# Kernel tuning notes

Hardware: AMD Instinct MI355X
Metric: run time of the kernel (lower is better)

Reference implementation:

```python
import jax, jax.numpy as jnp
import numpy as np

SIGMA = 0.1   # sigma_disc (params[3])
ALPHA = 0.05  # alpha_disc (params[2])


def setup_inputs() -> dict:
    key = jax.random.key(0)
    k1, k2, k3 = jax.random.split(key, 3)
    E, S, T = 3, 8192, 100  # num_events, num_samples, num_bin + num_extra_bin
    logits = jax.random.normal(k1, (E, S, T), dtype=jnp.float32)
    event_out = jax.nn.softmax(logits, axis=-1)  # per-event discrete hazard probs, rows sum to 1
    event_times = jax.random.randint(k2, (S, E), 0, 99).astype(jnp.int32)
    labs = jax.random.randint(k3, (S, E), 0, 2).astype(jnp.int32)
    return {"event_out": event_out, "event_times": event_times, "labs": labs,
            "num_bin": 96, "num_extra_bin": 4}


def _c_loss(event_out, event_times, labs, T):
    # cum[e, k, t] = sum(event_out[e, k, :t+1]); risk with cutoff c = 1 - cum[..., c-1]
    cum = jnp.cumsum(event_out, axis=-1)  # (E, S, T)
    E = event_out.shape[0]
    penalty = jnp.float32(0.0)
    for i in range(E):  # small fixed number of events
        c = cum[i]                    # (S, T)
        t = event_times[:, i]         # (S,)
        lab = labs[:, i]              # (S,)
        had = lab == 1
        # ---- forward concordance (had_event branch) ----
        e_f = jnp.minimum(t + 1, T - 1)              # per-reference-sample cutoff, >= 1
        # risk_f[j, k] = 1 - sum(event_out[k, :e_f[j]]) = 1 - cum[k, e_f[j]-1]
        risk_f = 1.0 - c[:, e_f - 1].T               # (S_j, S_k)
        diff_f = risk_f - jnp.diagonal(risk_f)[:, None]  # comp_risk - reference_risk
        # f_compare: t_k > e_j - 1  OR  (t_k == e_j - 1 AND lab_k == 0)
        mask_f = had[:, None] & ((t[None, :] >= e_f[:, None]) |
                                 ((t[None, :] == e_f[:, None] - 1) & (lab[None, :] == 0)))
        penalty = penalty + jnp.sum(jnp.where(mask_f & (diff_f < 0),
                                              jnp.exp(-diff_f / SIGMA), 0.0))
        # ---- backward concordance (back_c branch, active when t_j > 0) ----
        e_b = jnp.minimum(jnp.where(had, t, t + 1), T - 1)
        risk_b = 1.0 - c[:, jnp.maximum(e_b, 1) - 1].T
        diff_b = risk_b - jnp.diagonal(risk_b)[:, None]
        # b_compare: t_k <= e_j - 1 AND lab_k == 1
        mask_b = (t > 0)[:, None] & (t[None, :] <= e_b[:, None] - 1) & (lab[None, :] == 1)
        penalty = penalty + jnp.sum(jnp.where(mask_b & (diff_b > 0),
                                              jnp.exp(diff_b / SIGMA), 0.0))
    return ALPHA * penalty


def reference(event_out, event_times, labs, num_bin, num_extra_bin):
    return _c_loss(event_out, event_times, labs, num_bin + num_extra_bin)
```

## Files before the change

kernel.cpp:

```cpp
#include <hip/hip_runtime.h>

#define E_CONST 3
#define T_CONST 100
#define C10 10.0f
#define ALPHA_C 0.05f
#define SPLIT 4

__device__ inline int waveInclScan(int v, int lane) {
    #pragma unroll
    for (int off = 1; off < 64; off <<= 1) {
        int n = __shfl_up(v, off, 64);
        if (lane >= off) v += n;
    }
    return v;
}

__global__ __launch_bounds__(256) void combo_kernel(
    const float* __restrict__ event_out, const int* __restrict__ et,
    const int* __restrict__ labs, float* __restrict__ cumT,
    int* __restrict__ perm, int* __restrict__ permB,
    int* __restrict__ binStartA, int* __restrict__ b1endA,
    int prepBlocks, int S)
{
    __shared__ float tile[64][101];
    __shared__ int histK[2 * T_CONST];
    __shared__ int histB[T_CONST];
    __shared__ int cursK[2 * T_CONST];
    __shared__ int cursB[T_CONST];
    __shared__ int wsK[4], wsB[4];

    const int tid = threadIdx.x;

    if ((int)blockIdx.x < prepBlocks) {
        const int rowbase = (int)blockIdx.x * 64;
        const float4* __restrict__ src =
            reinterpret_cast<const float4*>(event_out) + (size_t)rowbase * 25;
        for (int idx = tid; idx < 64 * 25; idx += 256) {
            const float4 v = src[idx];
            const int r = idx / 25;
            const int c = idx - r * 25;
            float* d = &tile[r][c * 4];
            d[0] = v.x; d[1] = v.y; d[2] = v.z; d[3] = v.w;
        }
        __syncthreads();
        if (tid < 64) {
            float run = 0.f;
            #pragma unroll 4
            for (int c = 0; c < T_CONST; ++c) { run += tile[tid][c]; tile[tid][c] = run; }
        }
        __syncthreads();
        const int i  = rowbase / S;
        const int s0 = rowbase - i * S;
        float* __restrict__ dst = cumT + (size_t)i * T_CONST * S + s0;
        for (int idx = tid; idx < 64 * T_CONST; idx += 256) {
            const int t = idx >> 6;
            const int r = idx & 63;
            dst[(size_t)t * S + r] = tile[r][t];
        }
        return;
    }

    const int i = (int)blockIdx.x - prepBlocks;
    const int lane = tid & 63, wid = tid >> 6;

    for (int b = tid; b < 2 * T_CONST; b += 256) histK[b] = 0;
    for (int b = tid; b < T_CONST; b += 256) histB[b] = 0;
    __syncthreads();

    for (int s0 = tid; s0 < S; s0 += 1024) {
        const int sB = s0 + 256, sC = s0 + 512, sD = s0 + 768;
        const int tA = et[s0 * E_CONST + i];
        const int lA = labs[s0 * E_CONST + i];
        int tB = 0, lB = 0, tC = 0, lC = 0, tD = 0, lD = 0;
        if (sB < S) { tB = et[sB * E_CONST + i]; lB = labs[sB * E_CONST + i]; }
        if (sC < S) { tC = et[sC * E_CONST + i]; lC = labs[sC * E_CONST + i]; }
        if (sD < S) { tD = et[sD * E_CONST + i]; lD = labs[sD * E_CONST + i]; }
        atomicAdd(&histK[tA * 2 + (1 - lA)], 1); if (lA) atomicAdd(&histB[tA], 1);
        if (sB < S) { atomicAdd(&histK[tB * 2 + (1 - lB)], 1); if (lB) atomicAdd(&histB[tB], 1); }
        if (sC < S) { atomicAdd(&histK[tC * 2 + (1 - lC)], 1); if (lC) atomicAdd(&histB[tC], 1); }
        if (sD < S) { atomicAdd(&histK[tD * 2 + (1 - lD)], 1); if (lD) atomicAdd(&histB[tD], 1); }
    }
    __syncthreads();

    const int vK = (tid < 2 * T_CONST) ? histK[tid] : 0;
    int inclK = waveInclScan(vK, lane);
    const int vB = (tid < T_CONST) ? histB[tid] : 0;
    int inclB = waveInclScan(vB, lane);
    if (lane == 63) { wsK[wid] = inclK; wsB[wid] = inclB; }
    __syncthreads();
    int offK = 0, offB = 0;
    for (int w = 0; w < wid; ++w) { offK += wsK[w]; offB += wsB[w]; }
    inclK += offK; inclB += offB;
    const int exclK = inclK - vK;
    const int exclB = inclB - vB;

    if (tid < 2 * T_CONST) {
        cursK[tid] = exclK;
        binStartA[i * 2 * T_CONST + tid] = exclK;
    }
    if (tid < T_CONST) {
        cursB[tid] = exclB;
        b1endA[i * T_CONST + tid] = inclB;
    }
    __syncthreads();

    for (int s0 = tid; s0 < S; s0 += 1024) {
        const int sB = s0 + 256, sC = s0 + 512, sD = s0 + 768;
        const int tA = et[s0 * E_CONST + i];
        const int lA = labs[s0 * E_CONST + i];
        int tB = 0, lB = 0, tC = 0, lC = 0, tD = 0, lD = 0;
        if (sB < S) { tB = et[sB * E_CONST + i]; lB = labs[sB * E_CONST + i]; }
        if (sC < S) { tC = et[sC * E_CONST + i]; lC = labs[sC * E_CONST + i]; }
        if (sD < S) { tD = et[sD * E_CONST + i]; lD = labs[sD * E_CONST + i]; }

        int slot = atomicAdd(&cursK[tA * 2 + (1 - lA)], 1);
        perm[i * S + slot] = s0;
        if (lA) { const int sb = atomicAdd(&cursB[tA], 1); permB[i * S + sb] = s0; }
        if (sB < S) {
            slot = atomicAdd(&cursK[tB * 2 + (1 - lB)], 1);
            perm[i * S + slot] = sB;
            if (lB) { const int sb = atomicAdd(&cursB[tB], 1); permB[i * S + sb] = sB; }
        }
        if (sC < S) {
            slot = atomicAdd(&cursK[tC * 2 + (1 - lC)], 1);
            perm[i * S + slot] = sC;
            if (lC) { const int sb = atomicAdd(&cursB[tC], 1); permB[i * S + sb] = sC; }
        }
        if (sD < S) {
            slot = atomicAdd(&cursK[tD * 2 + (1 - lD)], 1);
            perm[i * S + slot] = sD;
            if (lD) { const int sb = atomicAdd(&cursB[tD], 1); permB[i * S + sb] = sD; }
        }
    }
}

__global__ __launch_bounds__(256) void grouppair_kernel(
    const float* __restrict__ cumT, const int* __restrict__ perm,
    const int* __restrict__ permB, const int* __restrict__ binStartA,
    const int* __restrict__ b1endA, float* __restrict__ partials, int S)
{
    __shared__ __align__(16) float elds[2048];
    __shared__ float wsum[4];
    const int tid = threadIdx.x;

    int x = (int)blockIdx.x;
    const int sp = x & (SPLIT - 1); x >>= 2;
    const int dir = x & 1;          x >>= 1;
    const int tt = x % T_CONST;
    const int i  = x / T_CONST;

    const int* __restrict__ bs = binStartA + i * 2 * T_CONST;
    int kbeg, kend, rbeg, rlen, colIdx;
    if (dir == 0) {
        const int t = tt;
        kbeg = bs[2 * t];
        kend = bs[2 * t + 1];
        rbeg = kend;
        rlen = S - rbeg;
        colIdx = t;
    } else {
        const int cb = (T_CONST - 2) - tt;
        if (cb < 0) { if (tid == 0) partials[blockIdx.x] = 0.f; return; }
        kbeg = (cb == 0) ? bs[2] : bs[2 * cb + 1];
        kend = bs[2 * cb + 3];
        rbeg = 0;
        rlen = b1endA[i * T_CONST + cb];
        colIdx = cb;
    }
    const int K = kend - kbeg;
    if (K <= 0 || rlen <= 0) { if (tid == 0) partials[blockIdx.x] = 0.f; return; }

    const int qbeg = rbeg + (rlen * sp) / SPLIT;
    const int qend = rbeg + (rlen * (sp + 1)) / SPLIT;
    const int qn   = qend - qbeg;
    const int qnp  = (qn + 3) & ~3;

    const float* __restrict__ col = cumT + ((size_t)i * T_CONST + colIdx) * S;
    const int* __restrict__ pidx = (dir == 0 ? perm : permB) + i * S;
    const float sgn = (dir == 0) ? C10 : -C10;

    for (int idx = tid; idx < qnp; idx += 256) {
        float e = 0.f;
        if (idx < qn) e = __expf(sgn * col[pidx[qbeg + idx]]);
        elds[idx] = e;
    }
    __syncthreads();

    const int kq = tid & 31;
    const int ep = tid >> 5;
    const int qn4 = qnp >> 2;
    const float4* __restrict__ e4 = reinterpret_cast<const float4*>(elds);
    const int permBase = i * S;
    float blocktot = 0.f;
    const int nkc = (K + 31) >> 5;

    for (int kc = 0; kc < nkc; ++kc) {
        const int j = kbeg + (kc << 5) + kq;
        float thr = 1e30f, factor = 0.f;
        if (j < kend) {
            const float tval = __expf(C10 * col[perm[permBase + j]]);
            if (dir == 0) { thr = tval;          factor = 1.0f / tval; }
            else          { thr = 1.0f / tval;   factor = tval; }
        }
        float acc = 0.f;
        for (int q = ep; q < qn4; q += 8) {
            const float4 v = e4[q];
            acc += (v.x > thr) ? v.x : 0.f;
            acc += (v.y > thr) ? v.y : 0.f;
            acc += (v.z > thr) ? v.z : 0.f;
            acc += (v.w > thr) ? v.w : 0.f;
        }
        blocktot += acc * factor;
    }

    for (int off = 32; off > 0; off >>= 1) blocktot += __shfl_down(blocktot, off, 64);
    const int lane = tid & 63, wid = tid >> 6;
    if (lane == 0) wsum[wid] = blocktot;
    __syncthreads();
    if (tid == 0) partials[blockIdx.x] = wsum[0] + wsum[1] + wsum[2] + wsum[3];
}

__global__ __launch_bounds__(1024) void reduce_kernel(
    const float* __restrict__ partials, int n, float* __restrict__ out)
{
    const int tid = threadIdx.x;
    float s0 = 0.f, s1 = 0.f, s2 = 0.f, s3 = 0.f;
    const int n4 = n & ~3;
    for (int idx = tid * 4; idx < n4; idx += 4096) {
        const float4 v = *reinterpret_cast<const float4*>(partials + idx);
        s0 += v.x; s1 += v.y; s2 += v.z; s3 += v.w;
    }
    for (int idx = n4 + tid; idx < n; idx += 1024) s0 += partials[idx];
    float sum = (s0 + s1) + (s2 + s3);
    for (int off = 32; off > 0; off >>= 1) sum += __shfl_down(sum, off, 64);
    __shared__ float wsum[16];
    const int lane = tid & 63, wd = tid >> 6;
    if (lane == 0) wsum[wd] = sum;
    __syncthreads();
    if (tid == 0) {
        float t = 0.f;
        for (int w = 0; w < 16; ++w) t += wsum[w];
        out[0] = ALPHA_C * t;
    }
}

__global__ __launch_bounds__(64) void prep_fb_kernel(
    const float* __restrict__ event_out, const int* __restrict__ et,
    const int* __restrict__ labs, float* __restrict__ cumT,
    int* __restrict__ tlA, int S)
{
    const int gid = blockIdx.x * 64 + threadIdx.x;
    const int i = gid / S;
    const int s = gid - i * S;
    const float4* __restrict__ row =
        reinterpret_cast<const float4*>(event_out + (size_t)gid * T_CONST);
    float* __restrict__ base = cumT + (size_t)i * T_CONST * S + s;
    float run = 0.f;
    #pragma unroll
    for (int c = 0; c < T_CONST / 4; ++c) {
        const float4 v = row[c];
        const float c0 = run + v.x;
        const float c1 = c0 + v.y;
        const float c2 = c1 + v.z;
        const float c3 = c2 + v.w;
        base[(size_t)(4 * c + 0) * S] = c0;
        base[(size_t)(4 * c + 1) * S] = c1;
        base[(size_t)(4 * c + 2) * S] = c2;
        base[(size_t)(4 * c + 3) * S] = c3;
        run = c3;
    }
    const int t   = et[s * E_CONST + i];
    const int lab = labs[s * E_CONST + i];
    tlA[i * S + s] = (t & 0xffff) | (lab << 16);
}

__global__ __launch_bounds__(256) void pair_fb_kernel(
    const float* __restrict__ cumT, const int* __restrict__ tlA,
    float* __restrict__ partials, int S)
{
    const int bx = blockIdx.x;
    const int i = bx / S;
    const int k = bx - i * S;
    const int base = i * S;
    const int tlk = tlA[base + k];
    const int t_k = tlk & 0xffff;
    const int lab_k = tlk >> 16;
    const bool doF = (lab_k == 1);
    const bool doB = (t_k > 0);
    float sum = 0.f;
    if (doF || doB) {
        const int cb = lab_k ? (t_k > 0 ? t_k - 1 : 0) : t_k;
        const float* __restrict__ colF = cumT + ((size_t)i * T_CONST + t_k) * S;
        const float* __restrict__ colB = cumT + ((size_t)i * T_CONST + cb)  * S;
        const float vf_k = colF[k];
        const float vb_k = colB[k];
        const int* __restrict__ tlp = tlA + base;
        for (int s = threadIdx.x; s < S; s += 256) {
            const int tls = tlp[s];
            const int t_s = tls & 0xffff;
            const int lab_s = tls >> 16;
            if (doF) {
                const float vs = colF[s];
                const bool c = (t_s > t_k) | ((t_s == t_k) & (lab_s == 0));
                if (c & (vs > vf_k)) sum += __expf((vs - vf_k) * C10);
            }
            if (doB) {
                const float vs = colB[s];
                const bool c = (t_s <= cb) & (lab_s == 1);
                if (c & (vb_k > vs)) sum += __expf((vb_k - vs) * C10);
            }
        }
    }
    for (int off = 32; off > 0; off >>= 1) sum += __shfl_down(sum, off, 64);
    __shared__ float wsum[4];
    const int lane = threadIdx.x & 63, wd = threadIdx.x >> 6;
    if (lane == 0) wsum[wd] = sum;
    __syncthreads();
    if (threadIdx.x == 0) partials[bx] = wsum[0] + wsum[1] + wsum[2] + wsum[3];
}

extern "C" void kernel_launch(void* const* d_in, const int* in_sizes, int n_in,
                              void* d_out, int out_size, void* d_ws, size_t ws_size,
                              hipStream_t stream)
{
    const float* event_out = (const float*)d_in[0];
    const int*   et        = (const int*)d_in[1];
    const int*   labsp     = (const int*)d_in[2];
    const int S = in_sizes[1] / E_CONST;

    const size_t colElems = (size_t)E_CONST * T_CONST * S;
    const size_t esElems  = (size_t)E_CONST * S;
    const int    gpBlocks = E_CONST * T_CONST * 2 * SPLIT;

    char* p = (char*)d_ws;
    float* cumT     = (float*)p; p += colElems * 4;
    int*   perm     = (int*)p;   p += esElems * 4;
    int*   permB    = (int*)p;   p += esElems * 4;
    int*   binStart = (int*)p;   p += (size_t)E_CONST * 2 * T_CONST * 4;
    int*   b1end    = (int*)p;   p += (size_t)E_CONST * T_CONST * 4;
    float* partials = (float*)p; p += (size_t)gpBlocks * 4;
    const size_t needed = (size_t)(p - (char*)d_ws);
    const size_t fallback_needed = colElems * 4 + esElems * 4 * 2;

    const int prepBlocks = (E_CONST * S) / 64;

    if (ws_size >= needed && (E_CONST * S) % 64 == 0) {
        hipLaunchKernelGGL(combo_kernel, dim3(prepBlocks + E_CONST), dim3(256), 0, stream,
                           event_out, et, labsp, cumT, perm, permB,
                           binStart, b1end, prepBlocks, S);
        hipLaunchKernelGGL(grouppair_kernel, dim3(gpBlocks), dim3(256), 0, stream,
                           cumT, perm, permB, binStart, b1end, partials, S);
        hipLaunchKernelGGL(reduce_kernel, dim3(1), dim3(1024), 0, stream,
                           partials, gpBlocks, (float*)d_out);
    } else if (ws_size >= fallback_needed) {
        const int nB = E_CONST * S;
        float* cumT2     = (float*)d_ws;
        int*   tlA2      = (int*)(cumT2 + colElems);
        float* partials2 = (float*)(tlA2 + esElems);
        hipLaunchKernelGGL(prep_fb_kernel, dim3(E_CONST * S / 64), dim3(64), 0, stream,
                           event_out, et, labsp, cumT2, tlA2, S);
        hipLaunchKernelGGL(pair_fb_kernel, dim3(nB), dim3(256), 0, stream,
                           cumT2, tlA2, partials2, S);
        hipLaunchKernelGGL(reduce_kernel, dim3(1), dim3(1024), 0, stream,
                           partials2, nB, (float*)d_out);
    }
}
```

Measured before the change: 114.4 us.

## Register-block four references per thread and fold final reduction into pair kernel

In the pair kernel each thread now compares four reference thresholds against every exp value it reads from LDS. This reuses each shared-memory load four times, but the k chunk grows from 32 to 128. The separate reduce kernel launch is replaced by a last-block reduction using an atomic counter that the prep kernel resets. The prep/combo kernel also moves to 512-thread blocks. The cost is that, with roughly 40 samples per bin, many of the 128 k slots are padding with a 1e30 threshold, so compare work per useful pair can rise.

```diff
diff --git a/kernel.cpp b/kernel.cpp
--- a/kernel.cpp
+++ b/kernel.cpp
@@ -15,27 +15,28 @@
     return v;
 }
 
-__global__ __launch_bounds__(256) void combo_kernel(
+__global__ __launch_bounds__(512) void combo_kernel(
     const float* __restrict__ event_out, const int* __restrict__ et,
     const int* __restrict__ labs, float* __restrict__ cumT,
     int* __restrict__ perm, int* __restrict__ permB,
     int* __restrict__ binStartA, int* __restrict__ b1endA,
-    int prepBlocks, int S)
+    int* __restrict__ cnt, int prepBlocks, int S)
 {
     __shared__ float tile[64][101];
     __shared__ int histK[2 * T_CONST];
     __shared__ int histB[T_CONST];
     __shared__ int cursK[2 * T_CONST];
     __shared__ int cursB[T_CONST];
-    __shared__ int wsK[4], wsB[4];
+    __shared__ int wsK[8], wsB[8];
 
     const int tid = threadIdx.x;
 
     if ((int)blockIdx.x < prepBlocks) {
+        if (blockIdx.x == 0 && tid == 0) *cnt = 0;
         const int rowbase = (int)blockIdx.x * 64;
         const float4* __restrict__ src =
             reinterpret_cast<const float4*>(event_out) + (size_t)rowbase * 25;
-        for (int idx = tid; idx < 64 * 25; idx += 256) {
+        for (int idx = tid; idx < 64 * 25; idx += 512) {
             const float4 v = src[idx];
             const int r = idx / 25;
             const int c = idx - r * 25;
@@ -52,7 +53,7 @@
         const int i  = rowbase / S;
         const int s0 = rowbase - i * S;
         float* __restrict__ dst = cumT + (size_t)i * T_CONST * S + s0;
-        for (int idx = tid; idx < 64 * T_CONST; idx += 256) {
+        for (int idx = tid; idx < 64 * T_CONST; idx += 512) {
             const int t = idx >> 6;
             const int r = idx & 63;
             dst[(size_t)t * S + r] = tile[r][t];
@@ -63,12 +64,12 @@
     const int i = (int)blockIdx.x - prepBlocks;
     const int lane = tid & 63, wid = tid >> 6;
 
-    for (int b = tid; b < 2 * T_CONST; b += 256) histK[b] = 0;
-    for (int b = tid; b < T_CONST; b += 256) histB[b] = 0;
-    __syncthreads();
-
-    for (int s0 = tid; s0 < S; s0 += 1024) {
-        const int sB = s0 + 256, sC = s0 + 512, sD = s0 + 768;
+    for (int b = tid; b < 2 * T_CONST; b += 512) histK[b] = 0;
+    for (int b = tid; b < T_CONST; b += 512) histB[b] = 0;
+    __syncthreads();
+
+    for (int s0 = tid; s0 < S; s0 += 2048) {
+        const int sB = s0 + 512, sC = s0 + 1024, sD = s0 + 1536;
         const int tA = et[s0 * E_CONST + i];
         const int lA = labs[s0 * E_CONST + i];
         int tB = 0, lB = 0, tC = 0, lC = 0, tD = 0, lD = 0;
@@ -104,8 +105,8 @@
     }
     __syncthreads();
 
-    for (int s0 = tid; s0 < S; s0 += 1024) {
-        const int sB = s0 + 256, sC = s0 + 512, sD = s0 + 768;
+    for (int s0 = tid; s0 < S; s0 += 2048) {
+        const int sB = s0 + 512, sC = s0 + 1024, sD = s0 + 1536;
         const int tA = et[s0 * E_CONST + i];
         const int lA = labs[s0 * E_CONST + i];
         int tB = 0, lB = 0, tC = 0, lC = 0, tD = 0, lD = 0;
@@ -137,10 +138,12 @@
 __global__ __launch_bounds__(256) void grouppair_kernel(
     const float* __restrict__ cumT, const int* __restrict__ perm,
     const int* __restrict__ permB, const int* __restrict__ binStartA,
-    const int* __restrict__ b1endA, float* __restrict__ partials, int S)
+    const int* __restrict__ b1endA, float* __restrict__ partials,
+    int* __restrict__ cnt, float* __restrict__ out, int S, int nBlocks)
 {
     __shared__ __align__(16) float elds[2048];
     __shared__ float wsum[4];
+    __shared__ int lastFlag;
     const int tid = threadIdx.x;
 
     int x = (int)blockIdx.x;
@@ -150,74 +153,111 @@
     const int i  = x / T_CONST;
 
     const int* __restrict__ bs = binStartA + i * 2 * T_CONST;
-    int kbeg, kend, rbeg, rlen, colIdx;
+    int kbeg = 0, kend = 0, rbeg = 0, rlen = 0, colIdx = 0;
+    bool active = true;
     if (dir == 0) {
-        const int t = tt;
-        kbeg = bs[2 * t];
-        kend = bs[2 * t + 1];
+        kbeg = bs[2 * tt];
+        kend = bs[2 * tt + 1];
         rbeg = kend;
         rlen = S - rbeg;
-        colIdx = t;
+        colIdx = tt;
     } else {
         const int cb = (T_CONST - 2) - tt;
-        if (cb < 0) { if (tid == 0) partials[blockIdx.x] = 0.f; return; }
-        kbeg = (cb == 0) ? bs[2] : bs[2 * cb + 1];
-        kend = bs[2 * cb + 3];
-        rbeg = 0;
-        rlen = b1endA[i * T_CONST + cb];
-        colIdx = cb;
+        if (cb < 0) active = false;
+        else {
+            kbeg = (cb == 0) ? bs[2] : bs[2 * cb + 1];
+            kend = bs[2 * cb + 3];
+            rbeg = 0;
+            rlen = b1endA[i * T_CONST + cb];
+            colIdx = cb;
+        }
     }
     const int K = kend - kbeg;
-    if (K <= 0 || rlen <= 0) { if (tid == 0) partials[blockIdx.x] = 0.f; return; }
-
-    const int qbeg = rbeg + (rlen * sp) / SPLIT;
-    const int qend = rbeg + (rlen * (sp + 1)) / SPLIT;
-    const int qn   = qend - qbeg;
-    const int qnp  = (qn + 3) & ~3;
-
-    const float* __restrict__ col = cumT + ((size_t)i * T_CONST + colIdx) * S;
-    const int* __restrict__ pidx = (dir == 0 ? perm : permB) + i * S;
-    const float sgn = (dir == 0) ? C10 : -C10;
-
-    for (int idx = tid; idx < qnp; idx += 256) {
-        float e = 0.f;
-        if (idx < qn) e = __expf(sgn * col[pidx[qbeg + idx]]);
-        elds[idx] = e;
-    }
-    __syncthreads();
-
-    const int kq = tid & 31;
-    const int ep = tid >> 5;
-    const int qn4 = qnp >> 2;
-    const float4* __restrict__ e4 = reinterpret_cast<const float4*>(elds);
-    const int permBase = i * S;
+    if (K <= 0 || rlen <= 0) active = false;
+
     float blocktot = 0.f;
-    const int nkc = (K + 31) >> 5;
-
-    for (int kc = 0; kc < nkc; ++kc) {
-        const int j = kbeg + (kc << 5) + kq;
-        float thr = 1e30f, factor = 0.f;
-        if (j < kend) {
-            const float tval = __expf(C10 * col[perm[permBase + j]]);
-            if (dir == 0) { thr = tval;          factor = 1.0f / tval; }
-            else          { thr = 1.0f / tval;   factor = tval; }
-        }
-        float acc = 0.f;
-        for (int q = ep; q < qn4; q += 8) {
-            const float4 v = e4[q];
-            acc += (v.x > thr) ? v.x : 0.f;
-            acc += (v.y > thr) ? v.y : 0.f;
-            acc += (v.z > thr) ? v.z : 0.f;
-            acc += (v.w > thr) ? v.w : 0.f;
-        }
-        blocktot += acc * factor;
+    if (active) {
+        const int qbeg = rbeg + (rlen * sp) / SPLIT;
+        const int qend = rbeg + (rlen * (sp + 1)) / SPLIT;
+        const int qn   = qend - qbeg;
+        const int qnp  = (qn + 3) & ~3;
+
+        const float* __restrict__ col = cumT + ((size_t)i * T_CONST + colIdx) * S;
+        const int* __restrict__ pidx = (dir == 0 ? perm : permB) + i * S;
+        const float sgn = (dir == 0) ? C10 : -C10;
+
+        for (int idx = tid; idx < qnp; idx += 256) {
+            float e = 0.f;
+            if (idx < qn) e = __expf(sgn * col[pidx[qbeg + idx]]);
+            elds[idx] = e;
+        }
+        __syncthreads();
+
+        const int kq4 = (tid & 31) * 4;
+        const int ep  = tid >> 5;
+        const int qn4 = qnp >> 2;
+        const float4* __restrict__ e4 = reinterpret_cast<const float4*>(elds);
+        const int permBase = i * S;
+        const int nkc = (K + 127) >> 7;
+
+        for (int kc = 0; kc < nkc; ++kc) {
+            const int jb = kbeg + (kc << 7) + kq4;
+            float thr0 = 1e30f, thr1 = 1e30f, thr2 = 1e30f, thr3 = 1e30f;
+            float f0 = 0.f, f1 = 0.f, f2 = 0.f, f3 = 0.f;
+            if (jb + 0 < kend) { const float tv = __expf(C10 * col[perm[permBase + jb + 0]]);
+                if (dir == 0) { thr0 = tv; f0 = 1.0f / tv; } else { thr0 = 1.0f / tv; f0 = tv; } }
+            if (jb + 1 < kend) { const float tv = __expf(C10 * col[perm[permBase + jb + 1]]);
+                if (dir == 0) { thr1 = tv; f1 = 1.0f / tv; } else { thr1 = 1.0f / tv; f1 = tv; } }
+            if (jb + 2 < kend) { const float tv = __expf(C10 * col[perm[permBase + jb + 2]]);
+                if (dir == 0) { thr2 = tv; f2 = 1.0f / tv; } else { thr2 = 1.0f / tv; f2 = tv; } }
+            if (jb + 3 < kend) { const float tv = __expf(C10 * col[perm[permBase + jb + 3]]);
+                if (dir == 0) { thr3 = tv; f3 = 1.0f / tv; } else { thr3 = 1.0f / tv; f3 = tv; } }
+
+            float a0 = 0.f, a1 = 0.f, a2 = 0.f, a3 = 0.f;
+            for (int q = ep; q < qn4; q += 8) {
+                const float4 v = e4[q];
+                a0 += (v.x > thr0) ? v.x : 0.f;
+                a0 += (v.y > thr0) ? v.y : 0.f;
+                a0 += (v.z > thr0) ? v.z : 0.f;
+                a0 += (v.w > thr0) ? v.w : 0.f;
+                a1 += (v.x > thr1) ? v.x : 0.f;
+                a1 += (v.y > thr1) ? v.y : 0.f;
+                a1 += (v.z > thr1) ? v.z : 0.f;
+                a1 += (v.w > thr1) ? v.w : 0.f;
+                a2 += (v.x > thr2) ? v.x : 0.f;
+                a2 += (v.y > thr2) ? v.y : 0.f;
+                a2 += (v.z > thr2) ? v.z : 0.f;
+                a2 += (v.w > thr2) ? v.w : 0.f;
+                a3 += (v.x > thr3) ? v.x : 0.f;
+                a3 += (v.y > thr3) ? v.y : 0.f;
+                a3 += (v.z > thr3) ? v.z : 0.f;
+                a3 += (v.w > thr3) ? v.w : 0.f;
+            }
+            blocktot += a0 * f0 + a1 * f1 + a2 * f2 + a3 * f3;
+        }
     }
 
     for (int off = 32; off > 0; off >>= 1) blocktot += __shfl_down(blocktot, off, 64);
     const int lane = tid & 63, wid = tid >> 6;
     if (lane == 0) wsum[wid] = blocktot;
     __syncthreads();
-    if (tid == 0) partials[blockIdx.x] = wsum[0] + wsum[1] + wsum[2] + wsum[3];
+    if (tid == 0) {
+        partials[blockIdx.x] = wsum[0] + wsum[1] + wsum[2] + wsum[3];
+        __threadfence();
+        const int prev = atomicAdd(cnt, 1);
+        lastFlag = (prev == nBlocks - 1) ? 1 : 0;
+    }
+    __syncthreads();
+    if (lastFlag) {
+        __threadfence();
+        float s0 = 0.f;
+        for (int idx = tid; idx < nBlocks; idx += 256) s0 += partials[idx];
+        float sum = s0;
+        for (int off = 32; off > 0; off >>= 1) sum += __shfl_down(sum, off, 64);
+        if (lane == 0) wsum[wid] = sum;
+        __syncthreads();
+        if (tid == 0) out[0] = ALPHA_C * (wsum[0] + wsum[1] + wsum[2] + wsum[3]);
+    }
 }
 
 __global__ __launch_bounds__(1024) void reduce_kernel(
@@ -339,19 +379,19 @@
     int*   binStart = (int*)p;   p += (size_t)E_CONST * 2 * T_CONST * 4;
     int*   b1end    = (int*)p;   p += (size_t)E_CONST * T_CONST * 4;
     float* partials = (float*)p; p += (size_t)gpBlocks * 4;
+    int*   cnt      = (int*)p;   p += 4;
     const size_t needed = (size_t)(p - (char*)d_ws);
     const size_t fallback_needed = colElems * 4 + esElems * 4 * 2;
 
     const int prepBlocks = (E_CONST * S) / 64;
 
     if (ws_size >= needed && (E_CONST * S) % 64 == 0) {
-        hipLaunchKernelGGL(combo_kernel, dim3(prepBlocks + E_CONST), dim3(256), 0, stream,
+        hipLaunchKernelGGL(combo_kernel, dim3(prepBlocks + E_CONST), dim3(512), 0, stream,
                            event_out, et, labsp, cumT, perm, permB,
-                           binStart, b1end, prepBlocks, S);
+                           binStart, b1end, cnt, prepBlocks, S);
         hipLaunchKernelGGL(grouppair_kernel, dim3(gpBlocks), dim3(256), 0, stream,
-                           cumT, perm, permB, binStart, b1end, partials, S);
-        hipLaunchKernelGGL(reduce_kernel, dim3(1), dim3(1024), 0, stream,
-                           partials, gpBlocks, (float*)d_out);
+                           cumT, perm, permB, binStart, b1end, partials,
+                           cnt, (float*)d_out, S, gpBlocks);
     } else if (ws_size >= fallback_needed) {
         const int nB = E_CONST * S;
         float* cumT2     = (float*)d_ws;
```

New measurement: 170.3 us. 1.49x slower.

## Filter comparison samples in-block instead of via a sorted permB gather

Applied to the files above, without the earlier changes.

The pair kernel no longer reads a contiguous sorted range through the permutation arrays. Each block now scans its fixed quarter of samples directly, tests the forward or backward compare mask from event times and labels, and compacts the matching exponentials into shared memory with a wave scan. This removes the permB scatter and the backward histogram from the prep kernel, and makes the column reads coalesced rather than gathered. The prep kernel moves to 512 threads. In exchange every block now reads all S/4 samples, which adds extra loads and exp work, and the fast path is restricted to S/SPLIT == 2048.

```diff
diff --git a/kernel.cpp b/kernel.cpp
--- a/kernel.cpp
+++ b/kernel.cpp
@@ -15,19 +15,16 @@
     return v;
 }
 
-__global__ __launch_bounds__(256) void combo_kernel(
+__global__ __launch_bounds__(512) void combo_kernel(
     const float* __restrict__ event_out, const int* __restrict__ et,
     const int* __restrict__ labs, float* __restrict__ cumT,
-    int* __restrict__ perm, int* __restrict__ permB,
-    int* __restrict__ binStartA, int* __restrict__ b1endA,
+    int* __restrict__ perm, int* __restrict__ binStartA,
     int prepBlocks, int S)
 {
     __shared__ float tile[64][101];
     __shared__ int histK[2 * T_CONST];
-    __shared__ int histB[T_CONST];
     __shared__ int cursK[2 * T_CONST];
-    __shared__ int cursB[T_CONST];
-    __shared__ int wsK[4], wsB[4];
+    __shared__ int wsK[8];
 
     const int tid = threadIdx.x;
 
@@ -35,7 +32,7 @@
         const int rowbase = (int)blockIdx.x * 64;
         const float4* __restrict__ src =
             reinterpret_cast<const float4*>(event_out) + (size_t)rowbase * 25;
-        for (int idx = tid; idx < 64 * 25; idx += 256) {
+        for (int idx = tid; idx < 64 * 25; idx += 512) {
             const float4 v = src[idx];
             const int r = idx / 25;
             const int c = idx - r * 25;
@@ -52,7 +49,7 @@
         const int i  = rowbase / S;
         const int s0 = rowbase - i * S;
         float* __restrict__ dst = cumT + (size_t)i * T_CONST * S + s0;
-        for (int idx = tid; idx < 64 * T_CONST; idx += 256) {
+        for (int idx = tid; idx < 64 * T_CONST; idx += 512) {
             const int t = idx >> 6;
             const int r = idx & 63;
             dst[(size_t)t * S + r] = tile[r][t];
@@ -63,49 +60,41 @@
     const int i = (int)blockIdx.x - prepBlocks;
     const int lane = tid & 63, wid = tid >> 6;
 
-    for (int b = tid; b < 2 * T_CONST; b += 256) histK[b] = 0;
-    for (int b = tid; b < T_CONST; b += 256) histB[b] = 0;
-    __syncthreads();
-
-    for (int s0 = tid; s0 < S; s0 += 1024) {
-        const int sB = s0 + 256, sC = s0 + 512, sD = s0 + 768;
+    for (int b = tid; b < 2 * T_CONST; b += 512) histK[b] = 0;
+    __syncthreads();
+
+    for (int s0 = tid; s0 < S; s0 += 2048) {
+        const int sB = s0 + 512, sC = s0 + 1024, sD = s0 + 1536;
         const int tA = et[s0 * E_CONST + i];
         const int lA = labs[s0 * E_CONST + i];
         int tB = 0, lB = 0, tC = 0, lC = 0, tD = 0, lD = 0;
         if (sB < S) { tB = et[sB * E_CONST + i]; lB = labs[sB * E_CONST + i]; }
         if (sC < S) { tC = et[sC * E_CONST + i]; lC = labs[sC * E_CONST + i]; }
         if (sD < S) { tD = et[sD * E_CONST + i]; lD = labs[sD * E_CONST + i]; }
-        atomicAdd(&histK[tA * 2 + (1 - lA)], 1); if (lA) atomicAdd(&histB[tA], 1);
-        if (sB < S) { atomicAdd(&histK[tB * 2 + (1 - lB)], 1); if (lB) atomicAdd(&histB[tB], 1); }
-        if (sC < S) { atomicAdd(&histK[tC * 2 + (1 - lC)], 1); if (lC) atomicAdd(&histB[tC], 1); }
-        if (sD < S) { atomicAdd(&histK[tD * 2 + (1 - lD)], 1); if (lD) atomicAdd(&histB[tD], 1); }
+        atomicAdd(&histK[tA * 2 + (1 - lA)], 1);
+        if (sB < S) atomicAdd(&histK[tB * 2 + (1 - lB)], 1);
+        if (sC < S) atomicAdd(&histK[tC * 2 + (1 - lC)], 1);
+        if (sD < S) atomicAdd(&histK[tD * 2 + (1 - lD)], 1);
     }
     __syncthreads();
 
     const int vK = (tid < 2 * T_CONST) ? histK[tid] : 0;
     int inclK = waveInclScan(vK, lane);
-    const int vB = (tid < T_CONST) ? histB[tid] : 0;
-    int inclB = waveInclScan(vB, lane);
-    if (lane == 63) { wsK[wid] = inclK; wsB[wid] = inclB; }
-    __syncthreads();
-    int offK = 0, offB = 0;
-    for (int w = 0; w < wid; ++w) { offK += wsK[w]; offB += wsB[w]; }
-    inclK += offK; inclB += offB;
+    if (lane == 63) wsK[wid] = inclK;
+    __syncthreads();
+    int offK = 0;
+    for (int w = 0; w < wid; ++w) offK += wsK[w];
+    inclK += offK;
     const int exclK = inclK - vK;
-    const int exclB = inclB - vB;
 
     if (tid < 2 * T_CONST) {
         cursK[tid] = exclK;
         binStartA[i * 2 * T_CONST + tid] = exclK;
     }
-    if (tid < T_CONST) {
-        cursB[tid] = exclB;
-        b1endA[i * T_CONST + tid] = inclB;
-    }
-    __syncthreads();
-
-    for (int s0 = tid; s0 < S; s0 += 1024) {
-        const int sB = s0 + 256, sC = s0 + 512, sD = s0 + 768;
+    __syncthreads();
+
+    for (int s0 = tid; s0 < S; s0 += 2048) {
+        const int sB = s0 + 512, sC = s0 + 1024, sD = s0 + 1536;
         const int tA = et[s0 * E_CONST + i];
         const int lA = labs[s0 * E_CONST + i];
         int tB = 0, lB = 0, tC = 0, lC = 0, tD = 0, lD = 0;
@@ -115,33 +104,23 @@
 
         int slot = atomicAdd(&cursK[tA * 2 + (1 - lA)], 1);
         perm[i * S + slot] = s0;
-        if (lA) { const int sb = atomicAdd(&cursB[tA], 1); permB[i * S + sb] = s0; }
-        if (sB < S) {
-            slot = atomicAdd(&cursK[tB * 2 + (1 - lB)], 1);
-            perm[i * S + slot] = sB;
-            if (lB) { const int sb = atomicAdd(&cursB[tB], 1); permB[i * S + sb] = sB; }
-        }
-        if (sC < S) {
-            slot = atomicAdd(&cursK[tC * 2 + (1 - lC)], 1);
-            perm[i * S + slot] = sC;
-            if (lC) { const int sb = atomicAdd(&cursB[tC], 1); permB[i * S + sb] = sC; }
-        }
-        if (sD < S) {
-            slot = atomicAdd(&cursK[tD * 2 + (1 - lD)], 1);
-            perm[i * S + slot] = sD;
-            if (lD) { const int sb = atomicAdd(&cursB[tD], 1); permB[i * S + sb] = sD; }
-        }
+        if (sB < S) { slot = atomicAdd(&cursK[tB * 2 + (1 - lB)], 1); perm[i * S + slot] = sB; }
+        if (sC < S) { slot = atomicAdd(&cursK[tC * 2 + (1 - lC)], 1); perm[i * S + slot] = sC; }
+        if (sD < S) { slot = atomicAdd(&cursK[tD * 2 + (1 - lD)], 1); perm[i * S + slot] = sD; }
     }
 }
 
 __global__ __launch_bounds__(256) void grouppair_kernel(
     const float* __restrict__ cumT, const int* __restrict__ perm,
-    const int* __restrict__ permB, const int* __restrict__ binStartA,
-    const int* __restrict__ b1endA, float* __restrict__ partials, int S)
+    const int* __restrict__ et, const int* __restrict__ labs,
+    const int* __restrict__ binStartA, float* __restrict__ partials, int S)
 {
     __shared__ __align__(16) float elds[2048];
     __shared__ float wsum[4];
+    __shared__ int wcnt[4];
+    __shared__ int nTot;
     const int tid = threadIdx.x;
+    const int lane = tid & 63, wid = tid >> 6;
 
     int x = (int)blockIdx.x;
     const int sp = x & (SPLIT - 1); x >>= 2;
@@ -150,71 +129,87 @@
     const int i  = x / T_CONST;
 
     const int* __restrict__ bs = binStartA + i * 2 * T_CONST;
-    int kbeg, kend, rbeg, rlen, colIdx;
+    int kbeg = 0, kend = 0, colIdx = 0, tref = 0;
+    bool active = true;
     if (dir == 0) {
-        const int t = tt;
-        kbeg = bs[2 * t];
-        kend = bs[2 * t + 1];
-        rbeg = kend;
-        rlen = S - rbeg;
-        colIdx = t;
+        kbeg = bs[2 * tt]; kend = bs[2 * tt + 1]; colIdx = tt; tref = tt;
     } else {
         const int cb = (T_CONST - 2) - tt;
-        if (cb < 0) { if (tid == 0) partials[blockIdx.x] = 0.f; return; }
-        kbeg = (cb == 0) ? bs[2] : bs[2 * cb + 1];
-        kend = bs[2 * cb + 3];
-        rbeg = 0;
-        rlen = b1endA[i * T_CONST + cb];
-        colIdx = cb;
+        if (cb < 0) active = false;
+        else { kbeg = (cb == 0) ? bs[2] : bs[2 * cb + 1]; kend = bs[2 * cb + 3];
+               colIdx = cb; tref = cb; }
     }
     const int K = kend - kbeg;
-    if (K <= 0 || rlen <= 0) { if (tid == 0) partials[blockIdx.x] = 0.f; return; }
-
-    const int qbeg = rbeg + (rlen * sp) / SPLIT;
-    const int qend = rbeg + (rlen * (sp + 1)) / SPLIT;
-    const int qn   = qend - qbeg;
-    const int qnp  = (qn + 3) & ~3;
-
-    const float* __restrict__ col = cumT + ((size_t)i * T_CONST + colIdx) * S;
-    const int* __restrict__ pidx = (dir == 0 ? perm : permB) + i * S;
-    const float sgn = (dir == 0) ? C10 : -C10;
-
-    for (int idx = tid; idx < qnp; idx += 256) {
-        float e = 0.f;
-        if (idx < qn) e = __expf(sgn * col[pidx[qbeg + idx]]);
-        elds[idx] = e;
-    }
-    __syncthreads();
-
-    const int kq = tid & 31;
-    const int ep = tid >> 5;
-    const int qn4 = qnp >> 2;
-    const float4* __restrict__ e4 = reinterpret_cast<const float4*>(elds);
-    const int permBase = i * S;
+    if (K <= 0) active = false;
+
     float blocktot = 0.f;
-    const int nkc = (K + 31) >> 5;
-
-    for (int kc = 0; kc < nkc; ++kc) {
-        const int j = kbeg + (kc << 5) + kq;
-        float thr = 1e30f, factor = 0.f;
-        if (j < kend) {
-            const float tval = __expf(C10 * col[perm[permBase + j]]);
-            if (dir == 0) { thr = tval;          factor = 1.0f / tval; }
-            else          { thr = 1.0f / tval;   factor = tval; }
-        }
-        float acc = 0.f;
-        for (int q = ep; q < qn4; q += 8) {
-            const float4 v = e4[q];
-            acc += (v.x > thr) ? v.x : 0.f;
-            acc += (v.y > thr) ? v.y : 0.f;
-            acc += (v.z > thr) ? v.z : 0.f;
-            acc += (v.w > thr) ? v.w : 0.f;
-        }
-        blocktot += acc * factor;
+    if (active) {
+        const int chunk = S / SPLIT;
+        const int cbeg = sp * chunk;
+        const float* __restrict__ col = cumT + ((size_t)i * T_CONST + colIdx) * S;
+        const float sgn = (dir == 0) ? C10 : -C10;
+
+        float ev[8];
+        int mask = 0, m = 0;
+        #pragma unroll
+        for (int j = 0; j < 8; ++j) {
+            const int s = cbeg + tid + j * 256;
+            const int ts = et[s * E_CONST + i];
+            const int ls = labs[s * E_CONST + i];
+            const bool mem = (dir == 0)
+                ? ((ts > tref) | ((ts == tref) & (ls == 0)))
+                : ((ts <= tref) & (ls == 1));
+            ev[j] = __expf(sgn * col[s]);
+            if (mem) { mask |= (1 << j); ++m; }
+        }
+        const int incl = waveInclScan(m, lane);
+        if (lane == 63) wcnt[wid] = incl;
+        __syncthreads();
+        int off = 0;
+        for (int w = 0; w < wid; ++w) off += wcnt[w];
+        int base = incl - m + off;
+        #pragma unroll
+        for (int j = 0; j < 8; ++j)
+            if (mask & (1 << j)) elds[base++] = ev[j];
+        if (tid == 255) {
+            const int n = base;
+            nTot = n;
+            const int np = (n + 3) & ~3;
+            for (int p = n; p < np; ++p) elds[p] = 0.f;
+        }
+        __syncthreads();
+
+        const int n = nTot;
+        if (n > 0) {
+            const int qn4 = ((n + 3) & ~3) >> 2;
+            const int kq = tid & 31;
+            const int ep = tid >> 5;
+            const float4* __restrict__ e4 = reinterpret_cast<const float4*>(elds);
+            const int permBase = i * S;
+            const int nkc = (K + 31) >> 5;
+
+            for (int kc = 0; kc < nkc; ++kc) {
+                const int j = kbeg + (kc << 5) + kq;
+                float thr = 1e30f, factor = 0.f;
+                if (j < kend) {
+                    const float tval = __expf(C10 * col[perm[permBase + j]]);
+                    if (dir == 0) { thr = tval;        factor = 1.0f / tval; }
+                    else          { thr = 1.0f / tval; factor = tval; }
+                }
+                float acc = 0.f;
+                for (int q = ep; q < qn4; q += 8) {
+                    const float4 v = e4[q];
+                    acc += (v.x > thr) ? v.x : 0.f;
+                    acc += (v.y > thr) ? v.y : 0.f;
+                    acc += (v.z > thr) ? v.z : 0.f;
+                    acc += (v.w > thr) ? v.w : 0.f;
+                }
+                blocktot += acc * factor;
+            }
+        }
     }
 
     for (int off = 32; off > 0; off >>= 1) blocktot += __shfl_down(blocktot, off, 64);
-    const int lane = tid & 63, wid = tid >> 6;
     if (lane == 0) wsum[wid] = blocktot;
     __syncthreads();
     if (tid == 0) partials[blockIdx.x] = wsum[0] + wsum[1] + wsum[2] + wsum[3];
@@ -335,21 +330,19 @@
     char* p = (char*)d_ws;
     float* cumT     = (float*)p; p += colElems * 4;
     int*   perm     = (int*)p;   p += esElems * 4;
-    int*   permB    = (int*)p;   p += esElems * 4;
     int*   binStart = (int*)p;   p += (size_t)E_CONST * 2 * T_CONST * 4;
-    int*   b1end    = (int*)p;   p += (size_t)E_CONST * T_CONST * 4;
     float* partials = (float*)p; p += (size_t)gpBlocks * 4;
     const size_t needed = (size_t)(p - (char*)d_ws);
     const size_t fallback_needed = colElems * 4 + esElems * 4 * 2;
 
     const int prepBlocks = (E_CONST * S) / 64;
 
-    if (ws_size >= needed && (E_CONST * S) % 64 == 0) {
-        hipLaunchKernelGGL(combo_kernel, dim3(prepBlocks + E_CONST), dim3(256), 0, stream,
-                           event_out, et, labsp, cumT, perm, permB,
-                           binStart, b1end, prepBlocks, S);
+    if (ws_size >= needed && (E_CONST * S) % 64 == 0 && (S / SPLIT) == 2048) {
+        hipLaunchKernelGGL(combo_kernel, dim3(prepBlocks + E_CONST), dim3(512), 0, stream,
+                           event_out, et, labsp, cumT, perm, binStart,
+                           prepBlocks, S);
         hipLaunchKernelGGL(grouppair_kernel, dim3(gpBlocks), dim3(256), 0, stream,
-                           cumT, perm, permB, binStart, b1end, partials, S);
+                           cumT, perm, et, labsp, binStart, partials, S);
         hipLaunchKernelGGL(reduce_kernel, dim3(1), dim3(1024), 0, stream,
                            partials, gpBlocks, (float*)d_out);
     } else if (ws_size >= fallback_needed) {
```

Measured after the change: 107.1 us. 6.4% less time.
